# Performance work log

Measured on AMD Instinct MI355X. Metric: run time of the kernel, lower is better.

## Reference

```python
import jax, jax.numpy as jnp
import numpy as np

N_NODES = 50000
N_EDGES = 800000
HIDDEN = 128
IN_DIM = 128
OUT_DIM = 1
N_LAYERS = 4
N_GRAPHS = 32
LN_EPS = 1e-5


def setup_inputs() -> dict:
    key = jax.random.key(0)
    ks = jax.random.split(key, 12)
    s = 1.0 / np.sqrt(HIDDEN)
    inp = {
        "x": jax.random.normal(ks[0], (N_NODES, IN_DIM), dtype=jnp.float32),
        "edge_index": jax.random.randint(ks[1], (2, N_EDGES), 0, N_NODES, dtype=jnp.int64),
        "batch": jnp.sort(jax.random.randint(ks[2], (N_NODES,), 0, N_GRAPHS, dtype=jnp.int64)),
        "W_emb": jax.random.normal(ks[3], (HIDDEN, IN_DIM), dtype=jnp.float32) * s,
        "b_emb": jax.random.normal(ks[4], (HIDDEN,), dtype=jnp.float32) * s,
        "W_layers": jax.random.normal(ks[5], (N_LAYERS, HIDDEN, HIDDEN), dtype=jnp.float32) * s,
        "b_layers": jax.random.normal(ks[6], (N_LAYERS, HIDDEN), dtype=jnp.float32) * s,
        "ln_gamma": 1.0 + 0.02 * jax.random.normal(ks[7], (N_LAYERS, HIDDEN), dtype=jnp.float32),
        "ln_beta": 0.02 * jax.random.normal(ks[8], (N_LAYERS, HIDDEN), dtype=jnp.float32),
        "W_out": jax.random.normal(ks[9], (OUT_DIM, HIDDEN), dtype=jnp.float32) * s,
    }
    return inp


def _layer_norm(x, gamma, beta):
    mu = jnp.mean(x, axis=-1, keepdims=True)
    var = jnp.mean(jnp.square(x - mu), axis=-1, keepdims=True)
    return (x - mu) * jax.lax.rsqrt(var + LN_EPS) * gamma + beta


def reference(x, edge_index, batch, W_emb, b_emb, W_layers, b_layers, ln_gamma, ln_beta, W_out):
    n = x.shape[0]
    # add self-loops (PyG GCNConv default)
    loop = jnp.arange(n, dtype=edge_index.dtype)
    row = jnp.concatenate([edge_index[0], loop])  # source nodes
    col = jnp.concatenate([edge_index[1], loop])  # target nodes
    # symmetric normalization: deg over targets
    deg = jax.ops.segment_sum(jnp.ones_like(col, dtype=x.dtype), col, num_segments=n)
    dis = jnp.where(deg > 0, jax.lax.rsqrt(jnp.maximum(deg, 1.0)), 0.0)
    norm = dis[row] * dis[col]  # [E+N]

    h = x @ W_emb.T + b_emb  # embedding layer
    for i in range(N_LAYERS):
        t = h @ W_layers[i].T                      # [N, H] linear first
        msg = t[row] * norm[:, None]               # gather + scale  [E+N, H]
        agg = jax.ops.segment_sum(msg, col, num_segments=n) + b_layers[i]
        h = _layer_norm(h + jax.nn.relu(agg), ln_gamma[i], ln_beta[i])

    out = h @ W_out.T                              # [N, OUT_DIM]
    sums = jax.ops.segment_sum(out, batch, num_segments=N_GRAPHS)
    cnts = jax.ops.segment_sum(jnp.ones((n,), out.dtype), batch, num_segments=N_GRAPHS)
    return sums / jnp.maximum(cnts, 1.0)[:, None]  # [N_GRAPHS, OUT_DIM]
```

## Files before the change

kernel.cpp:

```cpp
#include <hip/hip_runtime.h>
#include <hip/hip_fp16.h>

#define NN 50000
#define NE 800000
#define NH 128
#define NG 32
#define NL 4
#define NB 196
#define WSLOT (NH * NH)

typedef __attribute__((ext_vector_type(8))) short bf16x8;
typedef __attribute__((ext_vector_type(4))) float f32x4;
typedef __attribute__((ext_vector_type(2))) float f32x2;

__device__ inline short f2bf(float x) {
  union { float f; unsigned u; } v;
  v.f = x;
  unsigned r = v.u + 0x7FFF + ((v.u >> 16) & 1);
  return (short)(r >> 16);
}
__device__ inline float bf2f(short s) {
  union { unsigned u; float f; } v;
  v.u = ((unsigned)(unsigned short)s) << 16;
  return v.f;
}

__device__ inline int block_exscan(int v) {
  __shared__ int wsum[4];
  int tid = threadIdx.x, wave = tid >> 6, lane = tid & 63;
  int x = v;
#pragma unroll
  for (int off = 1; off < 64; off <<= 1) {
    int y = __shfl_up(x, off, 64);
    if (lane >= off) x += y;
  }
  if (lane == 63) wsum[wave] = x;
  __syncthreads();
  int wp = 0;
  if (wave > 0) wp += wsum[0];
  if (wave > 1) wp += wsum[1];
  if (wave > 2) wp += wsum[2];
  return wp + x - v;
}

__global__ __launch_bounds__(256) void prep_swizzle(const float* __restrict__ W_emb,
                                                    const float* __restrict__ W_layers,
                                                    short* __restrict__ hi,
                                                    short* __restrict__ lo) {
  int i = blockIdx.x * 256 + threadIdx.x;
  if (i >= 5 * WSLOT) return;
  int slot = i >> 14, f = i & (WSLOT - 1);
  int j = f & 7, lane = (f >> 3) & 63, tt = (f >> 9) & 7, ks = f >> 12;
  int n = tt * 16 + (lane & 15);
  int k = ks * 32 + ((lane >> 4) & 3) * 8 + j;
  const float* W = slot ? (W_layers + (size_t)(slot - 1) * WSLOT) : W_emb;
  float x = W[n * NH + k];
  short hh = f2bf(x);
  hi[i] = hh;
  lo[i] = f2bf(x - bf2f(hh));
}

__global__ __launch_bounds__(256) void hist_kernel(const int* __restrict__ col,
                                                   int* __restrict__ cnt,
                                                   int* __restrict__ rank) {
  int e = blockIdx.x * 256 + threadIdx.x;
  if (e < NE) rank[e] = atomicAdd(&cnt[col[e]], 1);
}

__global__ __launch_bounds__(256) void scan1_kernel(const int* __restrict__ cnt,
                                                    int* __restrict__ bsum,
                                                    float* __restrict__ dis) {
  int i = blockIdx.x * 256 + threadIdx.x;
  int v = (i < NN) ? cnt[i] : 0;
  if (i < NN) dis[i] = rsqrtf((float)(v + 1));
  int lane = threadIdx.x & 63;
  int s = v;
#pragma unroll
  for (int off = 32; off; off >>= 1) s += __shfl_down(s, off, 64);
  __shared__ int ws[4];
  if (lane == 0) ws[threadIdx.x >> 6] = s;
  __syncthreads();
  if (threadIdx.x == 0) bsum[blockIdx.x] = ws[0] + ws[1] + ws[2] + ws[3];
}

__global__ __launch_bounds__(256) void scan2_kernel(const int* __restrict__ bsum,
                                                    int* __restrict__ ebsum) {
  int tid = threadIdx.x;
  int v = (tid < NB) ? bsum[tid] : 0;
  int ex = block_exscan(v);
  if (tid < NB) ebsum[tid] = ex;
}

__global__ __launch_bounds__(256) void scan3_kernel(const int* __restrict__ cnt,
                                                    const int* __restrict__ ebsum,
                                                    int* __restrict__ offs) {
  int i = blockIdx.x * 256 + threadIdx.x;
  int v = (i < NN) ? cnt[i] : 0;
  int ex = block_exscan(v);
  if (i < NN) offs[i] = ebsum[blockIdx.x] + ex;
}

__global__ __launch_bounds__(256) void fill_kernel(const int* __restrict__ row,
                                                   const int* __restrict__ col,
                                                   const int* __restrict__ rank,
                                                   const float* __restrict__ dis,
                                                   const int* __restrict__ offs,
                                                   int2* __restrict__ csr) {
  int e = blockIdx.x * 256 + threadIdx.x;
  if (e < NE) {
    int d = col[e];
    int s = row[e];
    int pos = offs[d] + rank[e];
    csr[pos] = make_int2(s, __float_as_int(dis[s] * dis[d]));
  }
}

template <bool FP8_OUT>
__global__ __launch_bounds__(512) void gemm_mfma(const float* __restrict__ X,
                                                 const short* __restrict__ Whi,
                                                 const short* __restrict__ Wlo,
                                                 const float* __restrict__ bias,
                                                 float* __restrict__ Yf,
                                                 unsigned char* __restrict__ Y8) {
  __shared__ short Wh[WSLOT];
  __shared__ short Wl[WSLOT];
  int tid = threadIdx.x;
#pragma unroll
  for (int i = tid * 8; i < WSLOT; i += 512 * 8) {
    *(bf16x8*)&Wh[i] = *(const bf16x8*)(Whi + i);
    *(bf16x8*)&Wl[i] = *(const bf16x8*)(Wlo + i);
  }
  __syncthreads();

  int wave = tid >> 6, lane = tid & 63;
  int quad = lane >> 4, r16 = lane & 15;
  int m0 = blockIdx.x * 128 + wave * 16;
  if (m0 >= NN) return;
  int mA = m0 + r16;

  f32x4 acc[8];
#pragma unroll
  for (int t = 0; t < 8; ++t) acc[t] = (f32x4){0.f, 0.f, 0.f, 0.f};

#pragma unroll
  for (int ks = 0; ks < 4; ++ks) {
    int klane = ks * 32 + quad * 8;
    const float* xr = X + (size_t)mA * NH + klane;
    float4 a0 = *(const float4*)xr;
    float4 a1 = *(const float4*)(xr + 4);
    float af[8] = {a0.x, a0.y, a0.z, a0.w, a1.x, a1.y, a1.z, a1.w};
    bf16x8 xhi, xlo;
#pragma unroll
    for (int j = 0; j < 8; ++j) {
      short h = f2bf(af[j]);
      xhi[j] = h;
      xlo[j] = f2bf(af[j] - bf2f(h));
    }
#pragma unroll
    for (int t = 0; t < 8; ++t) {
      int fidx = ((ks * 8 + t) * 64 + lane) << 3;
      bf16x8 whi = *(const bf16x8*)&Wh[fidx];
      bf16x8 wlo = *(const bf16x8*)&Wl[fidx];
      if (FP8_OUT) {
        acc[t] = __builtin_amdgcn_mfma_f32_16x16x32_bf16(whi, xhi, acc[t], 0, 0, 0);
        acc[t] = __builtin_amdgcn_mfma_f32_16x16x32_bf16(whi, xlo, acc[t], 0, 0, 0);
        acc[t] = __builtin_amdgcn_mfma_f32_16x16x32_bf16(wlo, xhi, acc[t], 0, 0, 0);
      } else {
        acc[t] = __builtin_amdgcn_mfma_f32_16x16x32_bf16(xhi, whi, acc[t], 0, 0, 0);
        acc[t] = __builtin_amdgcn_mfma_f32_16x16x32_bf16(xlo, whi, acc[t], 0, 0, 0);
        acc[t] = __builtin_amdgcn_mfma_f32_16x16x32_bf16(xhi, wlo, acc[t], 0, 0, 0);
      }
    }
  }
  if (FP8_OUT) {
    unsigned* dst = (unsigned*)(Y8 + (size_t)(m0 + r16) * NH);
#pragma unroll
    for (int t = 0; t < 8; ++t) {
      int v = 0;
      v = __builtin_amdgcn_cvt_pk_fp8_f32(acc[t][0], acc[t][1], v, 0);
      v = __builtin_amdgcn_cvt_pk_fp8_f32(acc[t][2], acc[t][3], v, 1);
      dst[t * 4 + quad] = (unsigned)v;
    }
  } else {
    int mrow = m0 + quad * 4;
#pragma unroll
    for (int t = 0; t < 8; ++t) {
      int col = t * 16 + r16;
      float bb = bias ? bias[col] : 0.f;
#pragma unroll
      for (int r = 0; r < 4; ++r)
        Yf[(size_t)(mrow + r) * NH + col] = acc[t][r] + bb;
    }
  }
}

__global__ __launch_bounds__(256) void aggregate_kernel(
    const unsigned char* __restrict__ t8, float* __restrict__ h,
    const float* __restrict__ dis, const int* __restrict__ offs,
    const int* __restrict__ cnt, const int2* __restrict__ csr,
    const float* __restrict__ bias, const float* __restrict__ gamma,
    const float* __restrict__ beta, const float* __restrict__ Wout,
    float* __restrict__ nodeval) {
  int node = blockIdx.x * 4 + (threadIdx.x >> 6);
  int lane = threadIdx.x & 63;
  if (node >= NN) return;
  int hf = lane >> 5;
  int c32 = lane & 31;
  int c4 = c32 << 2;
  const unsigned* t32 = (const unsigned*)t8;

  float4 hv = *(const float4*)(h + (size_t)node * NH + c4);
  float4 bv = *(const float4*)(bias + c4);
  float4 gv = *(const float4*)(gamma + c4);
  float4 bt = *(const float4*)(beta + c4);
  float4 wv = make_float4(0.f, 0.f, 0.f, 0.f);
  if (Wout) wv = *(const float4*)(Wout + c4);

  float dii = dis[node];
  float sl = dii * dii;
  float4 a = make_float4(0.f, 0.f, 0.f, 0.f);
  if (hf == 0) {
    unsigned raw = t32[(size_t)node * 32 + c32];
    f32x2 lo2 = __builtin_amdgcn_cvt_pk_f32_fp8(raw, 0);
    f32x2 hi2 = __builtin_amdgcn_cvt_pk_f32_fp8(raw, 1);
    a.x = lo2.x * sl; a.y = lo2.y * sl; a.z = hi2.x * sl; a.w = hi2.y * sl;
  }
  int s0 = offs[node];
  int e = cnt[node];
  int j = 0;
  for (; j + 16 <= e; j += 16) {
    int2 p[8];
    unsigned raw[8];
#pragma unroll
    for (int u = 0; u < 8; ++u) p[u] = csr[s0 + j + 2 * u + hf];
#pragma unroll
    for (int u = 0; u < 8; ++u) raw[u] = t32[(size_t)p[u].x * 32 + c32];
#pragma unroll
    for (int u = 0; u < 8; ++u) {
      float w = __int_as_float(p[u].y);
      f32x2 lo2 = __builtin_amdgcn_cvt_pk_f32_fp8(raw[u], 0);
      f32x2 hi2 = __builtin_amdgcn_cvt_pk_f32_fp8(raw[u], 1);
      a.x += lo2.x * w; a.y += lo2.y * w; a.z += hi2.x * w; a.w += hi2.y * w;
    }
  }
  for (; j + 8 <= e; j += 8) {
    int2 p[4];
    unsigned raw[4];
#pragma unroll
    for (int u = 0; u < 4; ++u) p[u] = csr[s0 + j + 2 * u + hf];
#pragma unroll
    for (int u = 0; u < 4; ++u) raw[u] = t32[(size_t)p[u].x * 32 + c32];
#pragma unroll
    for (int u = 0; u < 4; ++u) {
      float w = __int_as_float(p[u].y);
      f32x2 lo2 = __builtin_amdgcn_cvt_pk_f32_fp8(raw[u], 0);
      f32x2 hi2 = __builtin_amdgcn_cvt_pk_f32_fp8(raw[u], 1);
      a.x += lo2.x * w; a.y += lo2.y * w; a.z += hi2.x * w; a.w += hi2.y * w;
    }
  }
  for (; j < e; j += 2) {
    int idx = j + hf;
    int2 p = (idx < e) ? csr[s0 + idx] : make_int2(node, 0);
    float w = __int_as_float(p.y);
    unsigned raw = t32[(size_t)p.x * 32 + c32];
    f32x2 lo2 = __builtin_amdgcn_cvt_pk_f32_fp8(raw, 0);
    f32x2 hi2 = __builtin_amdgcn_cvt_pk_f32_fp8(raw, 1);
    a.x += lo2.x * w; a.y += lo2.y * w; a.z += hi2.x * w; a.w += hi2.y * w;
  }
  a.x += __shfl_down(a.x, 32, 64);
  a.y += __shfl_down(a.y, 32, 64);
  a.z += __shfl_down(a.z, 32, 64);
  a.w += __shfl_down(a.w, 32, 64);
  float v0 = hv.x + fmaxf(a.x + bv.x, 0.f);
  float v1 = hv.y + fmaxf(a.y + bv.y, 0.f);
  float v2 = hv.z + fmaxf(a.z + bv.z, 0.f);
  float v3 = hv.w + fmaxf(a.w + bv.w, 0.f);
  float s = v0 + v1 + v2 + v3;
  float s2 = v0 * v0 + v1 * v1 + v2 * v2 + v3 * v3;
#pragma unroll
  for (int off = 16; off; off >>= 1) {
    s += __shfl_xor(s, off, 64);
    s2 += __shfl_xor(s2, off, 64);
  }
  float mean = s * (1.f / 128.f);
  float var = fmaxf(s2 * (1.f / 128.f) - mean * mean, 0.f);
  float inv = rsqrtf(var + 1e-5f);
  float4 o;
  o.x = (v0 - mean) * inv * gv.x + bt.x;
  o.y = (v1 - mean) * inv * gv.y + bt.y;
  o.z = (v2 - mean) * inv * gv.z + bt.z;
  o.w = (v3 - mean) * inv * gv.w + bt.w;
  if (lane < 32) *(float4*)(h + (size_t)node * NH + c4) = o;
  if (Wout) {
    float d = o.x * wv.x + o.y * wv.y + o.z * wv.z + o.w * wv.w;
#pragma unroll
    for (int off = 16; off; off >>= 1) d += __shfl_xor(d, off, 64);
    if (lane == 0) nodeval[node] = d;
  }
}

__global__ __launch_bounds__(256) void reduce_pool_kernel(
    const float* __restrict__ nodeval, const int* __restrict__ batch,
    float* __restrict__ gsum, int* __restrict__ gcnt) {
  __shared__ float bins[NG];
  __shared__ int cbins[NG];
  int tid = threadIdx.x;
  if (tid < NG) {
    bins[tid] = 0.f;
    cbins[tid] = 0;
  }
  __syncthreads();
  int i = blockIdx.x * 256 + tid;
  if (i < NN) {
    int g = batch[i];
    atomicAdd(&bins[g], nodeval[i]);
    atomicAdd(&cbins[g], 1);
  }
  __syncthreads();
  if (tid < NG) {
    if (cbins[tid]) {
      atomicAdd(&gsum[tid], bins[tid]);
      atomicAdd(&gcnt[tid], cbins[tid]);
    }
  }
}

__global__ void finalize_kernel(const float* __restrict__ gsum,
                                const int* __restrict__ gcnt,
                                float* __restrict__ out) {
  int g = threadIdx.x;
  if (g < NG) out[g] = gsum[g] / fmaxf((float)gcnt[g], 1.0f);
}

extern "C" void kernel_launch(void* const* d_in, const int* in_sizes, int n_in,
                              void* d_out, int out_size, void* d_ws, size_t ws_size,
                              hipStream_t stream) {
  const float* x = (const float*)d_in[0];
  const int* eidx = (const int*)d_in[1];
  const int* batch = (const int*)d_in[2];
  const float* W_emb = (const float*)d_in[3];
  const float* b_emb = (const float*)d_in[4];
  const float* W_layers = (const float*)d_in[5];
  const float* b_layers = (const float*)d_in[6];
  const float* ln_gamma = (const float*)d_in[7];
  const float* ln_beta = (const float*)d_in[8];
  const float* W_out = (const float*)d_in[9];
  float* out = (float*)d_out;

  char* ws = (char*)d_ws;
  unsigned char* t8 = (unsigned char*)ws; ws += (size_t)NN * NH;
  float* h = (float*)ws;        ws += (size_t)NN * NH * 4;
  short* Whi = (short*)ws;      ws += (size_t)5 * WSLOT * 2;
  short* Wlo = (short*)ws;      ws += (size_t)5 * WSLOT * 2;
  float* dis = (float*)ws;      ws += (size_t)NN * 4;
  int2* csr = (int2*)ws;        ws += (size_t)NE * 8;
  int* rank = (int*)ws;         ws += (size_t)NE * 4;
  int* offs = (int*)ws;         ws += (size_t)NN * 4;
  float* nodeval = (float*)ws;  ws += (size_t)NN * 4;
  int* bsum = (int*)ws;         ws += (size_t)NB * 4;
  int* ebsum = (int*)ws;        ws += (size_t)NB * 4;
  char* zero_base = ws;
  int* cnt = (int*)ws;          ws += (size_t)NN * 4;
  float* gsum = (float*)ws;     ws += (size_t)NG * 4;
  int* gcnt = (int*)ws;         ws += (size_t)NG * 4;
  size_t zero_bytes = (size_t)(ws - zero_base);
  hipMemsetAsync(zero_base, 0, zero_bytes, stream);

  const int* erow = eidx;
  const int* ecol = eidx + NE;

  prep_swizzle<<<(5 * WSLOT + 255) / 256, 256, 0, stream>>>(W_emb, W_layers, Whi,
                                                            Wlo);
  hist_kernel<<<(NE + 255) / 256, 256, 0, stream>>>(ecol, cnt, rank);
  scan1_kernel<<<NB, 256, 0, stream>>>(cnt, bsum, dis);
  scan2_kernel<<<1, 256, 0, stream>>>(bsum, ebsum);
  scan3_kernel<<<NB, 256, 0, stream>>>(cnt, ebsum, offs);
  fill_kernel<<<(NE + 255) / 256, 256, 0, stream>>>(erow, ecol, rank, dis, offs,
                                                    csr);
  int gblk = (NN + 127) / 128;
  gemm_mfma<false><<<gblk, 512, 0, stream>>>(x, Whi, Wlo, b_emb, h, nullptr);
  for (int l = 0; l < NL; ++l) {
    gemm_mfma<true><<<gblk, 512, 0, stream>>>(
        h, Whi + (size_t)(l + 1) * WSLOT, Wlo + (size_t)(l + 1) * WSLOT,
        nullptr, nullptr, t8);
    bool last = (l == NL - 1);
    aggregate_kernel<<<(NN + 3) / 4, 256, 0, stream>>>(
        t8, h, dis, offs, cnt, csr, b_layers + (size_t)l * NH,
        ln_gamma + (size_t)l * NH, ln_beta + (size_t)l * NH,
        last ? W_out : nullptr, nodeval);
  }
  reduce_pool_kernel<<<(NN + 255) / 256, 256, 0, stream>>>(nodeval, batch, gsum,
                                                           gcnt);
  finalize_kernel<<<1, 64, 0, stream>>>(gsum, gcnt, out);
}
```

Measured before the change: 403.3 us.

## Reorder to aggregate-then-transform and fuse residual LayerNorm into GEMM epilogue

Uses linearity to aggregate the fp8 node features first, then apply the linear layer, so the GEMM epilogue can fuse bias, ReLU, the residual add, LayerNorm and the output projection. Hidden state is stored as fp16 instead of fp32, and the aggregate result is written as fp16 for the GEMM to read. This moves the LayerNorm work out of the gather kernel and cuts bytes per node in both kernels. The trade-off is an extra fp16 agg buffer round trip, and fp8 quantization now applies to h before the matmul instead of after, which changes numerical error.

```diff
diff --git a/kernel.cpp b/kernel.cpp
--- a/kernel.cpp
+++ b/kernel.cpp
@@ -115,13 +115,19 @@
   }
 }
 
-template <bool FP8_OUT>
-__global__ __launch_bounds__(512) void gemm_mfma(const float* __restrict__ X,
+template <bool EMB, bool LAST>
+__global__ __launch_bounds__(512) void gemm_mfma(const float* __restrict__ Xf,
+                                                 const __half* __restrict__ Xh,
                                                  const short* __restrict__ Whi,
                                                  const short* __restrict__ Wlo,
                                                  const float* __restrict__ bias,
-                                                 float* __restrict__ Yf,
-                                                 unsigned char* __restrict__ Y8) {
+                                                 const __half* __restrict__ hprev,
+                                                 const float* __restrict__ gamma,
+                                                 const float* __restrict__ beta,
+                                                 const float* __restrict__ Wout,
+                                                 __half* __restrict__ hnew,
+                                                 unsigned char* __restrict__ h8,
+                                                 float* __restrict__ nodeval) {
   __shared__ short Wh[WSLOT];
   __shared__ short Wl[WSLOT];
   int tid = threadIdx.x;
@@ -145,10 +151,22 @@
 #pragma unroll
   for (int ks = 0; ks < 4; ++ks) {
     int klane = ks * 32 + quad * 8;
-    const float* xr = X + (size_t)mA * NH + klane;
-    float4 a0 = *(const float4*)xr;
-    float4 a1 = *(const float4*)(xr + 4);
-    float af[8] = {a0.x, a0.y, a0.z, a0.w, a1.x, a1.y, a1.z, a1.w};
+    float af[8];
+    if (EMB) {
+      const float* xr = Xf + (size_t)mA * NH + klane;
+      float4 a0 = *(const float4*)xr;
+      float4 a1 = *(const float4*)(xr + 4);
+      af[0] = a0.x; af[1] = a0.y; af[2] = a0.z; af[3] = a0.w;
+      af[4] = a1.x; af[5] = a1.y; af[6] = a1.z; af[7] = a1.w;
+    } else {
+      const __half2* xr = (const __half2*)(Xh + (size_t)mA * NH + klane);
+#pragma unroll
+      for (int q = 0; q < 4; ++q) {
+        float2 f = __half22float2(xr[q]);
+        af[2 * q] = f.x;
+        af[2 * q + 1] = f.y;
+      }
+    }
     bf16x8 xhi, xlo;
 #pragma unroll
     for (int j = 0; j < 8; ++j) {
@@ -161,61 +179,100 @@
       int fidx = ((ks * 8 + t) * 64 + lane) << 3;
       bf16x8 whi = *(const bf16x8*)&Wh[fidx];
       bf16x8 wlo = *(const bf16x8*)&Wl[fidx];
-      if (FP8_OUT) {
-        acc[t] = __builtin_amdgcn_mfma_f32_16x16x32_bf16(whi, xhi, acc[t], 0, 0, 0);
-        acc[t] = __builtin_amdgcn_mfma_f32_16x16x32_bf16(whi, xlo, acc[t], 0, 0, 0);
-        acc[t] = __builtin_amdgcn_mfma_f32_16x16x32_bf16(wlo, xhi, acc[t], 0, 0, 0);
+      acc[t] = __builtin_amdgcn_mfma_f32_16x16x32_bf16(whi, xhi, acc[t], 0, 0, 0);
+      acc[t] = __builtin_amdgcn_mfma_f32_16x16x32_bf16(whi, xlo, acc[t], 0, 0, 0);
+      acc[t] = __builtin_amdgcn_mfma_f32_16x16x32_bf16(wlo, xhi, acc[t], 0, 0, 0);
+    }
+  }
+
+  int m = m0 + r16;
+  int cb = quad * 4;
+  if (EMB) {
+#pragma unroll
+    for (int t = 0; t < 8; ++t) {
+      int ch = t * 16 + cb;
+      float4 bb = *(const float4*)(bias + ch);
+      float o0 = acc[t][0] + bb.x, o1 = acc[t][1] + bb.y;
+      float o2 = acc[t][2] + bb.z, o3 = acc[t][3] + bb.w;
+      __half2 p01 = __float22half2_rn(make_float2(o0, o1));
+      __half2 p23 = __float22half2_rn(make_float2(o2, o3));
+      *(uint2*)(hnew + (size_t)m * NH + ch) =
+          make_uint2(*(unsigned*)&p01, *(unsigned*)&p23);
+      int v = 0;
+      v = __builtin_amdgcn_cvt_pk_fp8_f32(o0, o1, v, 0);
+      v = __builtin_amdgcn_cvt_pk_fp8_f32(o2, o3, v, 1);
+      ((unsigned*)(h8 + (size_t)m * NH))[t * 4 + quad] = (unsigned)v;
+    }
+  } else {
+    float v[8][4];
+    float s = 0.f, s2 = 0.f;
+#pragma unroll
+    for (int t = 0; t < 8; ++t) {
+      int ch = t * 16 + cb;
+      float4 bb = *(const float4*)(bias + ch);
+      uint2 hp = *(const uint2*)(hprev + (size_t)m * NH + ch);
+      float2 h01 = __half22float2(*(__half2*)&hp.x);
+      float2 h23 = __half22float2(*(__half2*)&hp.y);
+      float hv[4] = {h01.x, h01.y, h23.x, h23.y};
+      float bb4[4] = {bb.x, bb.y, bb.z, bb.w};
+#pragma unroll
+      for (int r = 0; r < 4; ++r) {
+        float z = fmaxf(acc[t][r] + bb4[r], 0.f);
+        float val = hv[r] + z;
+        v[t][r] = val;
+        s += val;
+        s2 += val * val;
+      }
+    }
+    s += __shfl_xor(s, 16, 64);
+    s += __shfl_xor(s, 32, 64);
+    s2 += __shfl_xor(s2, 16, 64);
+    s2 += __shfl_xor(s2, 32, 64);
+    float mean = s * (1.f / 128.f);
+    float var = fmaxf(s2 * (1.f / 128.f) - mean * mean, 0.f);
+    float inv = rsqrtf(var + 1e-5f);
+    float d = 0.f;
+#pragma unroll
+    for (int t = 0; t < 8; ++t) {
+      int ch = t * 16 + cb;
+      float4 gv = *(const float4*)(gamma + ch);
+      float4 bt = *(const float4*)(beta + ch);
+      float o0 = (v[t][0] - mean) * inv * gv.x + bt.x;
+      float o1 = (v[t][1] - mean) * inv * gv.y + bt.y;
+      float o2 = (v[t][2] - mean) * inv * gv.z + bt.z;
+      float o3 = (v[t][3] - mean) * inv * gv.w + bt.w;
+      __half2 p01 = __float22half2_rn(make_float2(o0, o1));
+      __half2 p23 = __float22half2_rn(make_float2(o2, o3));
+      *(uint2*)(hnew + (size_t)m * NH + ch) =
+          make_uint2(*(unsigned*)&p01, *(unsigned*)&p23);
+      if (!LAST) {
+        int pv = 0;
+        pv = __builtin_amdgcn_cvt_pk_fp8_f32(o0, o1, pv, 0);
+        pv = __builtin_amdgcn_cvt_pk_fp8_f32(o2, o3, pv, 1);
+        ((unsigned*)(h8 + (size_t)m * NH))[t * 4 + quad] = (unsigned)pv;
       } else {
-        acc[t] = __builtin_amdgcn_mfma_f32_16x16x32_bf16(xhi, whi, acc[t], 0, 0, 0);
-        acc[t] = __builtin_amdgcn_mfma_f32_16x16x32_bf16(xlo, whi, acc[t], 0, 0, 0);
-        acc[t] = __builtin_amdgcn_mfma_f32_16x16x32_bf16(xhi, wlo, acc[t], 0, 0, 0);
+        float4 wv = *(const float4*)(Wout + ch);
+        d += o0 * wv.x + o1 * wv.y + o2 * wv.z + o3 * wv.w;
       }
     }
-  }
-  if (FP8_OUT) {
-    unsigned* dst = (unsigned*)(Y8 + (size_t)(m0 + r16) * NH);
-#pragma unroll
-    for (int t = 0; t < 8; ++t) {
-      int v = 0;
-      v = __builtin_amdgcn_cvt_pk_fp8_f32(acc[t][0], acc[t][1], v, 0);
-      v = __builtin_amdgcn_cvt_pk_fp8_f32(acc[t][2], acc[t][3], v, 1);
-      dst[t * 4 + quad] = (unsigned)v;
-    }
-  } else {
-    int mrow = m0 + quad * 4;
-#pragma unroll
-    for (int t = 0; t < 8; ++t) {
-      int col = t * 16 + r16;
-      float bb = bias ? bias[col] : 0.f;
-#pragma unroll
-      for (int r = 0; r < 4; ++r)
-        Yf[(size_t)(mrow + r) * NH + col] = acc[t][r] + bb;
+    if (LAST) {
+      d += __shfl_xor(d, 16, 64);
+      d += __shfl_xor(d, 32, 64);
+      if (lane < 16) nodeval[m] = d;
     }
   }
 }
 
 __global__ __launch_bounds__(256) void aggregate_kernel(
-    const unsigned char* __restrict__ t8, float* __restrict__ h,
+    const unsigned char* __restrict__ h8, __half* __restrict__ agg,
     const float* __restrict__ dis, const int* __restrict__ offs,
-    const int* __restrict__ cnt, const int2* __restrict__ csr,
-    const float* __restrict__ bias, const float* __restrict__ gamma,
-    const float* __restrict__ beta, const float* __restrict__ Wout,
-    float* __restrict__ nodeval) {
+    const int* __restrict__ cnt, const int2* __restrict__ csr) {
   int node = blockIdx.x * 4 + (threadIdx.x >> 6);
   int lane = threadIdx.x & 63;
   if (node >= NN) return;
   int hf = lane >> 5;
   int c32 = lane & 31;
-  int c4 = c32 << 2;
-  const unsigned* t32 = (const unsigned*)t8;
-
-  float4 hv = *(const float4*)(h + (size_t)node * NH + c4);
-  float4 bv = *(const float4*)(bias + c4);
-  float4 gv = *(const float4*)(gamma + c4);
-  float4 bt = *(const float4*)(beta + c4);
-  float4 wv = make_float4(0.f, 0.f, 0.f, 0.f);
-  if (Wout) wv = *(const float4*)(Wout + c4);
-
+  const unsigned* t32 = (const unsigned*)h8;
   float dii = dis[node];
   float sl = dii * dii;
   float4 a = make_float4(0.f, 0.f, 0.f, 0.f);
@@ -271,31 +328,11 @@
   a.y += __shfl_down(a.y, 32, 64);
   a.z += __shfl_down(a.z, 32, 64);
   a.w += __shfl_down(a.w, 32, 64);
-  float v0 = hv.x + fmaxf(a.x + bv.x, 0.f);
-  float v1 = hv.y + fmaxf(a.y + bv.y, 0.f);
-  float v2 = hv.z + fmaxf(a.z + bv.z, 0.f);
-  float v3 = hv.w + fmaxf(a.w + bv.w, 0.f);
-  float s = v0 + v1 + v2 + v3;
-  float s2 = v0 * v0 + v1 * v1 + v2 * v2 + v3 * v3;
-#pragma unroll
-  for (int off = 16; off; off >>= 1) {
-    s += __shfl_xor(s, off, 64);
-    s2 += __shfl_xor(s2, off, 64);
-  }
-  float mean = s * (1.f / 128.f);
-  float var = fmaxf(s2 * (1.f / 128.f) - mean * mean, 0.f);
-  float inv = rsqrtf(var + 1e-5f);
-  float4 o;
-  o.x = (v0 - mean) * inv * gv.x + bt.x;
-  o.y = (v1 - mean) * inv * gv.y + bt.y;
-  o.z = (v2 - mean) * inv * gv.z + bt.z;
-  o.w = (v3 - mean) * inv * gv.w + bt.w;
-  if (lane < 32) *(float4*)(h + (size_t)node * NH + c4) = o;
-  if (Wout) {
-    float d = o.x * wv.x + o.y * wv.y + o.z * wv.z + o.w * wv.w;
-#pragma unroll
-    for (int off = 16; off; off >>= 1) d += __shfl_xor(d, off, 64);
-    if (lane == 0) nodeval[node] = d;
+  if (lane < 32) {
+    __half2 p01 = __float22half2_rn(make_float2(a.x, a.y));
+    __half2 p23 = __float22half2_rn(make_float2(a.z, a.w));
+    *(uint2*)(agg + (size_t)node * NH + (c32 << 2)) =
+        make_uint2(*(unsigned*)&p01, *(unsigned*)&p23);
   }
 }
 
@@ -348,8 +385,9 @@
   float* out = (float*)d_out;
 
   char* ws = (char*)d_ws;
-  unsigned char* t8 = (unsigned char*)ws; ws += (size_t)NN * NH;
-  float* h = (float*)ws;        ws += (size_t)NN * NH * 4;
+  unsigned char* h8 = (unsigned char*)ws; ws += (size_t)NN * NH;
+  __half* h = (__half*)ws;      ws += (size_t)NN * NH * 2;
+  __half* agg = (__half*)ws;    ws += (size_t)NN * NH * 2;
   short* Whi = (short*)ws;      ws += (size_t)5 * WSLOT * 2;
   short* Wlo = (short*)ws;      ws += (size_t)5 * WSLOT * 2;
   float* dis = (float*)ws;      ws += (size_t)NN * 4;
@@ -378,16 +416,23 @@
   fill_kernel<<<(NE + 255) / 256, 256, 0, stream>>>(erow, ecol, rank, dis, offs,
                                                     csr);
   int gblk = (NN + 127) / 128;
-  gemm_mfma<false><<<gblk, 512, 0, stream>>>(x, Whi, Wlo, b_emb, h, nullptr);
+  gemm_mfma<true, false><<<gblk, 512, 0, stream>>>(
+      x, nullptr, Whi, Wlo, b_emb, nullptr, nullptr, nullptr, nullptr, h, h8,
+      nullptr);
   for (int l = 0; l < NL; ++l) {
-    gemm_mfma<true><<<gblk, 512, 0, stream>>>(
-        h, Whi + (size_t)(l + 1) * WSLOT, Wlo + (size_t)(l + 1) * WSLOT,
-        nullptr, nullptr, t8);
-    bool last = (l == NL - 1);
-    aggregate_kernel<<<(NN + 3) / 4, 256, 0, stream>>>(
-        t8, h, dis, offs, cnt, csr, b_layers + (size_t)l * NH,
-        ln_gamma + (size_t)l * NH, ln_beta + (size_t)l * NH,
-        last ? W_out : nullptr, nodeval);
+    aggregate_kernel<<<(NN + 3) / 4, 256, 0, stream>>>(h8, agg, dis, offs, cnt,
+                                                       csr);
+    const short* wh = Whi + (size_t)(l + 1) * WSLOT;
+    const short* wl = Wlo + (size_t)(l + 1) * WSLOT;
+    const float* bl = b_layers + (size_t)l * NH;
+    const float* gl = ln_gamma + (size_t)l * NH;
+    const float* be = ln_beta + (size_t)l * NH;
+    if (l == NL - 1)
+      gemm_mfma<false, true><<<gblk, 512, 0, stream>>>(
+          nullptr, agg, wh, wl, bl, h, gl, be, W_out, h, h8, nodeval);
+    else
+      gemm_mfma<false, false><<<gblk, 512, 0, stream>>>(
+          nullptr, agg, wh, wl, bl, h, gl, be, nullptr, h, h8, nullptr);
   }
   reduce_pool_kernel<<<(NN + 255) / 256, 256, 0, stream>>>(nodeval, batch, gsum,
                                                            gcnt);
```

Measured after the change: 377.2 us. -6.5%, faster.
